# Optimization experiments

Hardware: AMD Instinct MI355X
Metric: run time of the kernel (lower is better)

Reference implementation:

```python
import jax, jax.numpy as jnp
import numpy as np

B = 16384
D_IN = 1024
D_OUT = 512
H1 = 4 * D_IN      # floor(layersDimentions[0]*inputDimention) = 4096
H3 = 4 * D_OUT     # floor(layersDimentions[1]*outputDimention) = 2048
H4 = 4 * D_OUT     # floor(layersDimentions[2]*outputDimention) = 2048
M = 256            # codebook size


def _linear_params(key, fan_in, fan_out):
    kw, kb = jax.random.split(key)
    bound = 1.0 / np.sqrt(fan_in)
    w = jax.random.uniform(kw, (fan_out, fan_in), jnp.float32, -bound, bound)
    b = jax.random.uniform(kb, (fan_out,), jnp.float32, -bound, bound)
    return w, b


def setup_inputs() -> dict:
    key = jax.random.key(0)
    ks = jax.random.split(key, 7)
    x = jax.random.normal(ks[0], (B, D_IN), jnp.float32)
    codebook = jnp.sort(jax.random.normal(ks[1], (M,), jnp.float32))
    w1, b1 = _linear_params(ks[2], D_IN, H1)
    w2, b2 = _linear_params(ks[3], H1, D_OUT)
    w3, b3 = _linear_params(ks[4], D_OUT, H3)
    w4, b4 = _linear_params(ks[5], H3, H4)
    w5, b5 = _linear_params(ks[6], H4, D_OUT)
    return {"x": x, "codebook": codebook,
            "w1": w1, "b1": b1, "w2": w2, "b2": b2,
            "w3": w3, "b3": b3, "w4": w4, "b4": b4,
            "w5": w5, "b5": b5}


def _quantize(x, codebook):
    # nearest codeword per scalar element: argmin_m |x - c_m|
    # x: [B, D], codebook: [M]
    d = jnp.abs(x[..., None] - codebook)          # [B, D, M]
    idx = jnp.argmin(d, axis=-1)                  # [B, D]
    return codebook[idx]


def reference(x, codebook, w1, b1, w2, b2, w3, b3, w4, b4, w5, b5):
    h = x @ w1.T + b1                # [B, H1]
    h = h @ w2.T + b2                # [B, D_OUT]
    h = _quantize(h, codebook)       # [B, D_OUT]
    h = h @ w3.T + b3                # [B, H3]
    h = h @ w4.T + b4                # [B, H4]
    return h @ w5.T + b5             # [B, D_OUT]
```

## Files before the change

### kernel.cpp

```cpp
#include <hip/hip_runtime.h>


typedef __bf16 v8bf __attribute__((ext_vector_type(8)));
typedef float  v4f  __attribute__((ext_vector_type(4)));

#define Bdim   16384
#define DIN    1024
#define DOUT   512
#define H1dim  4096
#define H3dim  2048
#define H4dim  2048

#define GLOBAL_AS __attribute__((address_space(1)))
#define LDS_AS    __attribute__((address_space(3)))

__device__ __forceinline__ void load16_to_lds(const __bf16* g, __bf16* l) {
  __builtin_amdgcn_global_load_lds((const GLOBAL_AS unsigned int*)g,
                                   (LDS_AS unsigned int*)l, 16, 0, 0);
}

__device__ __forceinline__ unsigned pack2bf(float a, float b) {
  return (unsigned)__builtin_bit_cast(unsigned short, (__bf16)a) |
         ((unsigned)__builtin_bit_cast(unsigned short, (__bf16)b) << 16);
}

__device__ __forceinline__ void transpose_body(const float* __restrict__ in,
                                               __bf16* __restrict__ out,
                                               int R, int C, int bx, int by,
                                               float (*tile)[68]) {
  const int c0 = bx * 32, r0 = by * 64;
  const int t = threadIdx.x, tr = t >> 5, tc = t & 31;
#pragma unroll
  for (int i = 0; i < 8; ++i)
    tile[tc][tr + i * 8] = in[(size_t)(r0 + tr + i * 8) * C + (c0 + tc)];
  __syncthreads();
  const int orow = t >> 3, oc = (t & 7) * 8;
  float4 a = *(const float4*)&tile[orow][oc];
  float4 b = *(const float4*)&tile[orow][oc + 4];
  int4 o;
  o.x = pack2bf(a.x, a.y); o.y = pack2bf(a.z, a.w);
  o.z = pack2bf(b.x, b.y); o.w = pack2bf(b.z, b.w);
  *(int4*)&out[(size_t)(c0 + orow) * R + (r0 + oc)] = o;
}

__device__ __forceinline__ void cast16_body(const float* __restrict__ in,
                                            __bf16* __restrict__ out, int b) {
  const int t = threadIdx.x;
  const size_t base = (size_t)b * 4096;
#pragma unroll
  for (int c = 0; c < 4; ++c) {
    const size_t i = base + c * 1024 + t * 4;
    float4 v = *(const float4*)&in[i];
    uint2 o;
    o.x = pack2bf(v.x, v.y);
    o.y = pack2bf(v.z, v.w);
    *(uint2*)&out[i] = o;
  }
}

__global__ void prepw_kernel(const float* __restrict__ w1, __bf16* __restrict__ w1T,
                             const float* __restrict__ w4, __bf16* __restrict__ w4T,
                             const float* __restrict__ w2, __bf16* __restrict__ w2b,
                             const float* __restrict__ w5, __bf16* __restrict__ w5b) {
  __shared__ float tile[32][68];
  int b = blockIdx.x;
  if (b < 2048) {
    transpose_body(w1, w1T, H1dim, DIN, b & 31, b >> 5, tile);
  } else if (b < 4096) {
    b -= 2048;
    transpose_body(w4, w4T, H4dim, H3dim, b & 63, b >> 6, tile);
  } else if (b < 4608) {
    cast16_body(w2, w2b, b - 4096);
  } else {
    cast16_body(w5, w5b, b - 4608);
  }
}

__device__ __forceinline__ void bias_ba_body(int bb, const float* __restrict__ b1,
                                             const float* __restrict__ w2,
                                             const float* __restrict__ b2,
                                             float* __restrict__ ba) {
  const int wave = threadIdx.x >> 6, lane = threadIdx.x & 63;
  const int j = bb * 4 + wave;
  float s = 0.f;
  for (int k = lane; k < H1dim; k += 64) s += b1[k] * w2[(size_t)j * H1dim + k];
#pragma unroll
  for (int off = 32; off; off >>= 1) s += __shfl_xor(s, off, 64);
  if (lane == 0) ba[j] = s + b2[j];
}

__device__ __forceinline__ void bias_bc_body(int bb, const float* __restrict__ b3,
                                             const __bf16* __restrict__ WtT,
                                             const float* __restrict__ b4,
                                             const float* __restrict__ w5,
                                             const float* __restrict__ b5,
                                             float* __restrict__ bc) {
  const int wave = threadIdx.x >> 6, lane = threadIdx.x & 63;
  const int j = bb * 4 + wave;
  float s = 0.f;
  for (int k = lane; k < H4dim; k += 64)
    s += b3[k] * (float)WtT[(size_t)j * H4dim + k] + b4[k] * w5[(size_t)j * H4dim + k];
#pragma unroll
  for (int off = 32; off; off >>= 1) s += __shfl_xor(s, off, 64);
  if (lane == 0) bc[j] = s + b5[j];
}

enum { MODE_W = 0, MODE_Q = 1, MODE_OUT = 2 };

#define ASM_BAR() asm volatile("s_barrier" ::: "memory")

template <int MODE, int BM>
__device__ __forceinline__ void gemm_body(__bf16* As, __bf16* Bs, float* cbs,
                                          int bx, int by,
                                          const __bf16* __restrict__ A,
                                          const __bf16* __restrict__ Bt,
                                          void* __restrict__ Cout,
                                          const float* __restrict__ bias,
                                          const float* __restrict__ codebook,
                                          int M, int N, int K, int CH) {
  const int t = threadIdx.x;
  const int m0 = bx * BM, n0 = by * 64;
  if constexpr (MODE == MODE_Q) cbs[t] = codebook[t];

  const int lane = t & 63, wave = t >> 6;
  const int quad = lane >> 4, l15 = lane & 15;
  constexpr int MI = BM / 32;
  const int wm = (wave & 1) * (BM / 2), wn = (wave >> 1) * 32;

  const int lrow = lane >> 3;
  const int gcol = ((lane & 7) ^ lrow) * 8;
  const __bf16* gA = A  + (size_t)(m0 + (BM / 4) * wave + lrow) * K + gcol;
  const __bf16* gB = Bt + (size_t)(n0 + 16 * wave + lrow) * K + gcol;
  const int swz = l15 & 7;

  v4f acc[MI][2], accT[MI][2];
#pragma unroll
  for (int i = 0; i < MI; ++i)
#pragma unroll
    for (int j = 0; j < 2; ++j) {
      acc[i][j] = (v4f){0.f, 0.f, 0.f, 0.f};
      if constexpr (MODE == MODE_W) accT[i][j] = (v4f){0.f, 0.f, 0.f, 0.f};
    }

  auto stage = [&](int k0, int buf) {
    __bf16* lA = As + buf * (BM * 64) + (BM / 4) * wave * 64;
    __bf16* lB = Bs + buf * (64 * 64) + 16 * wave * 64;
#pragma unroll
    for (int p = 0; p < MI; ++p)
      load16_to_lds(gA + (size_t)(8 * p) * K + k0, lA + p * 512);
#pragma unroll
    for (int p = 0; p < 2; ++p)
      load16_to_lds(gB + (size_t)(8 * p) * K + k0, lB + p * 512);
  };

  const int nk = K >> 6;
  const int chsteps = CH >> 6;
  stage(0, 0);
  stage(64, 1);

  int cc = 0;
  for (int tk = 0; tk < nk; ++tk) {
    if (tk + 1 < nk) {
      if constexpr (BM == 128) asm volatile("s_waitcnt vmcnt(6)" ::: "memory");
      else                     asm volatile("s_waitcnt vmcnt(4)" ::: "memory");
    } else {
      asm volatile("s_waitcnt vmcnt(0)" ::: "memory");
    }
    ASM_BAR();

    const __bf16* cA = As + (tk & 1) * (BM * 64);
    const __bf16* cB = Bs + (tk & 1) * (64 * 64);
#pragma unroll
    for (int kk = 0; kk < 2; ++kk) {
      const int cch = ((kk * 4 + quad) ^ swz) * 8;
      v8bf af[MI], bv[2];
#pragma unroll
      for (int i = 0; i < MI; ++i)
        af[i] = *(const v8bf*)&cA[(wm + i * 16 + l15) * 64 + cch];
#pragma unroll
      for (int j = 0; j < 2; ++j)
        bv[j] = *(const v8bf*)&cB[(wn + j * 16 + l15) * 64 + cch];
#pragma unroll
      for (int i = 0; i < MI; ++i)
#pragma unroll
        for (int j = 0; j < 2; ++j)
          acc[i][j] = __builtin_amdgcn_mfma_f32_16x16x32_bf16(af[i], bv[j], acc[i][j], 0, 0, 0);
    }
    if constexpr (MODE == MODE_W) {
      if (++cc == chsteps) {
        cc = 0;
#pragma unroll
        for (int i = 0; i < MI; ++i)
#pragma unroll
          for (int j = 0; j < 2; ++j) {
            accT[i][j] += acc[i][j];
            acc[i][j] = (v4f){0.f, 0.f, 0.f, 0.f};
          }
      }
    }
    asm volatile("s_waitcnt lgkmcnt(0)" ::: "memory");
    ASM_BAR();
    if (tk + 2 < nk) stage((tk + 2) << 6, tk & 1);
  }

#pragma unroll
  for (int j = 0; j < 2; ++j) {
    const int gn = n0 + wn + j * 16 + l15;
    float bj = 0.f;
    if constexpr (MODE != MODE_W) bj = bias[gn];
#pragma unroll
    for (int i = 0; i < MI; ++i) {
#pragma unroll
      for (int r = 0; r < 4; ++r) {
        const int gm = m0 + wm + i * 16 + quad * 4 + r;
        if constexpr (MODE == MODE_W) {
          ((__bf16*)Cout)[(size_t)gm * N + gn] = (__bf16)accT[i][j][r];
        } else if constexpr (MODE == MODE_Q) {
          float v = acc[i][j][r] + bj;
          int idx = 0;
#pragma unroll
          for (int s = 128; s > 0; s >>= 1) {
            const int u = idx + s;
            if (cbs[u] <= v) idx = u;
          }
          float best = cbs[idx];
          if (idx < 255) {
            const float c1 = cbs[idx + 1];
            if (!(v - best <= c1 - v)) best = c1;
          }
          ((__bf16*)Cout)[(size_t)gm * N + gn] = (__bf16)best;
        } else {
          ((float*)Cout)[(size_t)gm * N + gn] = acc[i][j][r] + bj;
        }
      }
    }
  }
}

__global__ __launch_bounds__(256, 3)
void foldA_kernel(const __bf16* __restrict__ w2b, const __bf16* __restrict__ w1T,
                  __bf16* __restrict__ WaT,
                  const __bf16* __restrict__ w5b, const __bf16* __restrict__ w4T,
                  __bf16* __restrict__ WtT,
                  const float* __restrict__ b1, const float* __restrict__ w2,
                  const float* __restrict__ b2, float* __restrict__ ba,
                  const float* __restrict__ w3, __bf16* __restrict__ w3T,
                  const float* __restrict__ x, __bf16* __restrict__ xb) {
  __shared__ __align__(16) __bf16 As[2 * 64 * 64];
  __shared__ __align__(16) __bf16 Bs[2 * 64 * 64];
  __shared__ float tile[32][68];
  int b = blockIdx.x;
  if (b < 128) {
    const int c = b & 7, i = b >> 3;
    gemm_body<MODE_W, 64>(As, Bs, nullptr, i >> 1, c * 2 + (i & 1), w2b, w1T, WaT,
                          nullptr, nullptr, DOUT, DIN, H1dim, 512);
  } else if (b < 384) {
    b -= 128;
    const int c = b & 7, i = b >> 3;
    gemm_body<MODE_W, 64>(As, Bs, nullptr, i >> 2, c * 4 + (i & 3), w5b, w4T, WtT,
                          nullptr, nullptr, DOUT, H3dim, H4dim, 512);
  } else if (b < 512) {
    bias_ba_body(b - 384, b1, w2, b2, ba);
  } else if (b < 1024) {
    b -= 512;
    transpose_body(w3, w3T, H3dim, DOUT, b & 15, b >> 4, tile);
  } else {
    cast16_body(x, xb, b - 1024);
  }
}

__global__ __launch_bounds__(256, 3)
void foldB_kernel(const __bf16* __restrict__ WtT, const __bf16* __restrict__ w3T,
                  __bf16* __restrict__ WcT,
                  const float* __restrict__ b3, const float* __restrict__ b4,
                  const float* __restrict__ w5, const float* __restrict__ b5,
                  float* __restrict__ bc,
                  const __bf16* __restrict__ xb, const __bf16* __restrict__ WaT,
                  __bf16* __restrict__ q, const float* __restrict__ ba,
                  const float* __restrict__ cb) {
  __shared__ __align__(16) __bf16 As[2 * 128 * 64];
  __shared__ __align__(16) __bf16 Bs[2 * 64 * 64];
  __shared__ float cbs[256];
  int b = blockIdx.x;
  if (b < 64) {
    const int c = b & 7, i = b >> 3;
    gemm_body<MODE_W, 64>(As, Bs, nullptr, i, c, WtT, w3T, WcT,
                          nullptr, nullptr, DOUT, DOUT, H3dim, 256);
  } else if (b < 192) {
    bias_bc_body(b - 64, b3, WtT, b4, w5, b5, bc);
  } else {
    b -= 192;
    const int c = b & 7, i = b >> 3;
    gemm_body<MODE_Q, 128>(As, Bs, cbs, c * 16 + (i >> 3), i & 7, xb, WaT, q,
                           ba, cb, Bdim, DOUT, DIN, DIN);
  }
}

__global__ __launch_bounds__(256, 3)
void gemmout_kernel(const __bf16* __restrict__ q, const __bf16* __restrict__ WcT,
                    float* __restrict__ out, const float* __restrict__ bc) {
  __shared__ __align__(16) __bf16 As[2 * 128 * 64];
  __shared__ __align__(16) __bf16 Bs[2 * 64 * 64];
  const int b = blockIdx.x;
  const int c = b & 7, i = b >> 3;
  gemm_body<MODE_OUT, 128>(As, Bs, nullptr, c * 16 + (i >> 3), i & 7,
                           q, WcT, out, bc, nullptr, Bdim, DOUT, DOUT, DOUT);
}

extern "C" void kernel_launch(void* const* d_in, const int* in_sizes, int n_in,
                              void* d_out, int out_size, void* d_ws, size_t ws_size,
                              hipStream_t stream) {
  const float* x  = (const float*)d_in[0];
  const float* cb = (const float*)d_in[1];
  const float* w1 = (const float*)d_in[2];
  const float* b1 = (const float*)d_in[3];
  const float* w2 = (const float*)d_in[4];
  const float* b2 = (const float*)d_in[5];
  const float* w3 = (const float*)d_in[6];
  const float* b3 = (const float*)d_in[7];
  const float* w4 = (const float*)d_in[8];
  const float* b4 = (const float*)d_in[9];
  const float* w5 = (const float*)d_in[10];
  const float* b5 = (const float*)d_in[11];
  float* out = (float*)d_out;

  char* ws = (char*)d_ws;
  size_t off = 0;
  auto alloc = [&](size_t bytes) -> void* {
    void* p = ws + off;
    off = (off + bytes + 255) & ~(size_t)255;
    return p;
  };
  __bf16* w1T = (__bf16*)alloc((size_t)DIN * H1dim * 2);
  __bf16* w4T = (__bf16*)alloc((size_t)H3dim * H4dim * 2);
  __bf16* w3T = (__bf16*)alloc((size_t)DOUT * H3dim * 2);
  __bf16* w2b = (__bf16*)alloc((size_t)DOUT * H1dim * 2);
  __bf16* w5b = (__bf16*)alloc((size_t)DOUT * H4dim * 2);
  __bf16* WaT = (__bf16*)alloc((size_t)DOUT * DIN * 2);
  __bf16* WtT = (__bf16*)alloc((size_t)DOUT * H3dim * 2);
  __bf16* WcT = (__bf16*)alloc((size_t)DOUT * DOUT * 2);
  __bf16* q   = (__bf16*)alloc((size_t)Bdim * DOUT * 2);
  __bf16* xb  = (__bf16*)alloc((size_t)Bdim * DIN * 2);
  float*  ba  = (float*)alloc(DOUT * 4);
  float*  bc  = (float*)alloc(DOUT * 4);

  prepw_kernel<<<4864, 256, 0, stream>>>(w1, w1T, w4, w4T, w2, w2b, w5, w5b);

  foldA_kernel<<<5120, 256, 0, stream>>>(w2b, w1T, WaT, w5b, w4T, WtT,
                                         b1, w2, b2, ba, w3, w3T, x, xb);

  foldB_kernel<<<1216, 256, 0, stream>>>(WtT, w3T, WcT, b3, b4, w5, b5, bc,
                                         xb, WaT, q, ba, cb);

  gemmout_kernel<<<1024, 256, 0, stream>>>(q, WcT, out, bc);
}
```

Baseline: 253.6 us.

## Halve GEMM K-tile to 32 to shrink LDS and double occupancy

The shared GEMM body now stages 32-wide K slices instead of 64, with a new 4-column XOR swizzle and one MFMA step per barrier. LDS per block is cut roughly in half and the separate shared arrays are merged into one aliased buffer, so launch bounds go from 3 to 6 blocks per CU. The aim is more resident waves to hide memory latency. In exchange, each tile does half the MFMA work per barrier pair, so synchronisation and loop overhead grow relative to compute.

```diff
diff --git a/kernel.cpp b/kernel.cpp
--- a/kernel.cpp
+++ b/kernel.cpp
@@ -125,13 +125,13 @@
   const int lane = t & 63, wave = t >> 6;
   const int quad = lane >> 4, l15 = lane & 15;
   constexpr int MI = BM / 32;
+  constexpr int AP = BM / 64;
   const int wm = (wave & 1) * (BM / 2), wn = (wave >> 1) * 32;
 
-  const int lrow = lane >> 3;
-  const int gcol = ((lane & 7) ^ lrow) * 8;
-  const __bf16* gA = A  + (size_t)(m0 + (BM / 4) * wave + lrow) * K + gcol;
-  const __bf16* gB = Bt + (size_t)(n0 + 16 * wave + lrow) * K + gcol;
-  const int swz = l15 & 7;
+  const int srow = lane >> 2;
+  const int scol = (((lane & 3) ^ (srow & 3)) * 8);
+  const __bf16* gA = A  + (size_t)(m0 + (BM / 4) * wave + srow) * K + scol;
+  const __bf16* gB = Bt + (size_t)(n0 + 16 * wave + srow) * K + scol;
 
   v4f acc[MI][2], accT[MI][2];
 #pragma unroll
@@ -143,49 +143,45 @@
     }
 
   auto stage = [&](int k0, int buf) {
-    __bf16* lA = As + buf * (BM * 64) + (BM / 4) * wave * 64;
-    __bf16* lB = Bs + buf * (64 * 64) + 16 * wave * 64;
-#pragma unroll
-    for (int p = 0; p < MI; ++p)
-      load16_to_lds(gA + (size_t)(8 * p) * K + k0, lA + p * 512);
-#pragma unroll
-    for (int p = 0; p < 2; ++p)
-      load16_to_lds(gB + (size_t)(8 * p) * K + k0, lB + p * 512);
+    __bf16* lA = As + buf * (BM * 32) + (BM / 4) * wave * 32;
+    __bf16* lB = Bs + buf * (64 * 32) + 16 * wave * 32;
+#pragma unroll
+    for (int p = 0; p < AP; ++p)
+      load16_to_lds(gA + (size_t)(16 * p) * K + k0, lA + p * 512);
+    load16_to_lds(gB + k0, lB);
   };
 
-  const int nk = K >> 6;
-  const int chsteps = CH >> 6;
+  const int nk = K >> 5;
+  const int chsteps = CH >> 5;
   stage(0, 0);
-  stage(64, 1);
+  stage(32, 1);
 
   int cc = 0;
   for (int tk = 0; tk < nk; ++tk) {
     if (tk + 1 < nk) {
-      if constexpr (BM == 128) asm volatile("s_waitcnt vmcnt(6)" ::: "memory");
-      else                     asm volatile("s_waitcnt vmcnt(4)" ::: "memory");
+      if constexpr (BM == 128) asm volatile("s_waitcnt vmcnt(3)" ::: "memory");
+      else                     asm volatile("s_waitcnt vmcnt(2)" ::: "memory");
     } else {
       asm volatile("s_waitcnt vmcnt(0)" ::: "memory");
     }
     ASM_BAR();
 
-    const __bf16* cA = As + (tk & 1) * (BM * 64);
-    const __bf16* cB = Bs + (tk & 1) * (64 * 64);
-#pragma unroll
-    for (int kk = 0; kk < 2; ++kk) {
-      const int cch = ((kk * 4 + quad) ^ swz) * 8;
-      v8bf af[MI], bv[2];
-#pragma unroll
-      for (int i = 0; i < MI; ++i)
-        af[i] = *(const v8bf*)&cA[(wm + i * 16 + l15) * 64 + cch];
+    const __bf16* cA = As + (tk & 1) * (BM * 32);
+    const __bf16* cB = Bs + (tk & 1) * (64 * 32);
+    const int cch = (quad ^ (l15 & 3)) * 8;
+    v8bf af[MI], bv[2];
+#pragma unroll
+    for (int i = 0; i < MI; ++i)
+      af[i] = *(const v8bf*)&cA[(wm + i * 16 + l15) * 32 + cch];
+#pragma unroll
+    for (int j = 0; j < 2; ++j)
+      bv[j] = *(const v8bf*)&cB[(wn + j * 16 + l15) * 32 + cch];
+#pragma unroll
+    for (int i = 0; i < MI; ++i)
 #pragma unroll
       for (int j = 0; j < 2; ++j)
-        bv[j] = *(const v8bf*)&cB[(wn + j * 16 + l15) * 64 + cch];
-#pragma unroll
-      for (int i = 0; i < MI; ++i)
-#pragma unroll
-        for (int j = 0; j < 2; ++j)
-          acc[i][j] = __builtin_amdgcn_mfma_f32_16x16x32_bf16(af[i], bv[j], acc[i][j], 0, 0, 0);
-    }
+        acc[i][j] = __builtin_amdgcn_mfma_f32_16x16x32_bf16(af[i], bv[j], acc[i][j], 0, 0, 0);
+
     if constexpr (MODE == MODE_W) {
       if (++cc == chsteps) {
         cc = 0;
@@ -200,7 +196,7 @@
     }
     asm volatile("s_waitcnt lgkmcnt(0)" ::: "memory");
     ASM_BAR();
-    if (tk + 2 < nk) stage((tk + 2) << 6, tk & 1);
+    if (tk + 2 < nk) stage((tk + 2) << 5, tk & 1);
   }
 
 #pragma unroll
@@ -237,7 +233,7 @@
   }
 }
 
-__global__ __launch_bounds__(256, 3)
+__global__ __launch_bounds__(256, 6)
 void foldA_kernel(const __bf16* __restrict__ w2b, const __bf16* __restrict__ w1T,
                   __bf16* __restrict__ WaT,
                   const __bf16* __restrict__ w5b, const __bf16* __restrict__ w4T,
@@ -246,9 +242,9 @@
                   const float* __restrict__ b2, float* __restrict__ ba,
                   const float* __restrict__ w3, __bf16* __restrict__ w3T,
                   const float* __restrict__ x, __bf16* __restrict__ xb) {
-  __shared__ __align__(16) __bf16 As[2 * 64 * 64];
-  __shared__ __align__(16) __bf16 Bs[2 * 64 * 64];
-  __shared__ float tile[32][68];
+  __shared__ __align__(16) char smem[16384];
+  __bf16* As = (__bf16*)smem;
+  __bf16* Bs = (__bf16*)(smem + 8192);
   int b = blockIdx.x;
   if (b < 128) {
     const int c = b & 7, i = b >> 3;
@@ -263,13 +259,14 @@
     bias_ba_body(b - 384, b1, w2, b2, ba);
   } else if (b < 1024) {
     b -= 512;
-    transpose_body(w3, w3T, H3dim, DOUT, b & 15, b >> 4, tile);
+    transpose_body(w3, w3T, H3dim, DOUT, b & 15, b >> 4,
+                   reinterpret_cast<float(*)[68]>(smem));
   } else {
     cast16_body(x, xb, b - 1024);
   }
 }
 
-__global__ __launch_bounds__(256, 3)
+__global__ __launch_bounds__(256, 6)
 void foldB_kernel(const __bf16* __restrict__ WtT, const __bf16* __restrict__ w3T,
                   __bf16* __restrict__ WcT,
                   const float* __restrict__ b3, const float* __restrict__ b4,
@@ -278,11 +275,12 @@
                   const __bf16* __restrict__ xb, const __bf16* __restrict__ WaT,
                   __bf16* __restrict__ q, const float* __restrict__ ba,
                   const float* __restrict__ cb) {
-  __shared__ __align__(16) __bf16 As[2 * 128 * 64];
-  __shared__ __align__(16) __bf16 Bs[2 * 64 * 64];
+  __shared__ __align__(16) char smem[24576];
   __shared__ float cbs[256];
   int b = blockIdx.x;
   if (b < 64) {
+    __bf16* As = (__bf16*)smem;
+    __bf16* Bs = (__bf16*)(smem + 8192);
     const int c = b & 7, i = b >> 3;
     gemm_body<MODE_W, 64>(As, Bs, nullptr, i, c, WtT, w3T, WcT,
                           nullptr, nullptr, DOUT, DOUT, H3dim, 256);
@@ -290,17 +288,20 @@
     bias_bc_body(b - 64, b3, WtT, b4, w5, b5, bc);
   } else {
     b -= 192;
+    __bf16* As = (__bf16*)smem;
+    __bf16* Bs = (__bf16*)(smem + 16384);
     const int c = b & 7, i = b >> 3;
     gemm_body<MODE_Q, 128>(As, Bs, cbs, c * 16 + (i >> 3), i & 7, xb, WaT, q,
                            ba, cb, Bdim, DOUT, DIN, DIN);
   }
 }
 
-__global__ __launch_bounds__(256, 3)
+__global__ __launch_bounds__(256, 6)
 void gemmout_kernel(const __bf16* __restrict__ q, const __bf16* __restrict__ WcT,
                     float* __restrict__ out, const float* __restrict__ bc) {
-  __shared__ __align__(16) __bf16 As[2 * 128 * 64];
-  __shared__ __align__(16) __bf16 Bs[2 * 64 * 64];
+  __shared__ __align__(16) char smem[24576];
+  __bf16* As = (__bf16*)smem;
+  __bf16* Bs = (__bf16*)(smem + 16384);
   const int b = blockIdx.x;
   const int c = b & 7, i = b >> 3;
   gemm_body<MODE_OUT, 128>(As, Bs, nullptr, c * 16 + (i >> 3), i & 7,
```

Measured after the change: 262.6 us. +3.6%, slower.
